# Kernel tuning notes

Measured on AMD Instinct MI355X. Metric: run time of the kernel, lower is better.

The kernel has to match this reference:

```python
import jax, jax.numpy as jnp
import numpy as np

NEG = -1e9
BN_EPS = 1e-3  # keras BatchNormalization default epsilon
LRELU = 0.2    # GAT leaky-relu slope


def _gat(Xt, bias_mat, Wg, a1, a2, bg):
    """Dense multi-head GAT (Velickovic TF impl).
    Xt: [B,N,F], bias_mat: [B,N,N] additive mask (0 / -1e9).
    Wg: [H,F,D], a1/a2/bg: [H,D]. Returns [B,N,H*D]."""
    feats = jnp.einsum('bnf,hfd->bhnd', Xt, Wg)          # [B,H,N,D]
    f1 = jnp.einsum('bhnd,hd->bhn', feats, a1)
    f2 = jnp.einsum('bhnd,hd->bhn', feats, a2)
    logits = f1[:, :, :, None] + f2[:, :, None, :]        # [B,H,N,N]
    logits = jax.nn.leaky_relu(logits, LRELU) + bias_mat[:, None]
    coefs = jax.nn.softmax(logits, axis=-1)
    vals = jnp.einsum('bhnm,bhmd->bhnd', coefs, feats) + bg[None, :, None, :]
    vals = jax.nn.elu(vals)
    B, H, N, D = vals.shape
    return jnp.transpose(vals, (0, 2, 1, 3)).reshape(B, N, H * D)


def setup_inputs() -> dict:
    key = jax.random.key(0)
    ks = jax.random.split(key, 16)
    B, T, N, F = 4, 12, 2048, 64
    H, D = 4, 16           # attn_heads, hid_units
    C = H * D              # out_channels = 64

    X = jax.random.normal(ks[0], (B, T, N, F), dtype=jnp.float32)
    # random sparse adjacency (~avg degree 16) + self loops -> additive mask
    adj = jax.random.uniform(ks[1], (B, N, N)) < (16.0 / N)
    adj = adj | jnp.eye(N, dtype=bool)[None]
    bias_mat = jnp.where(adj, 0.0, NEG).astype(jnp.float32)

    he = lambda k, s: jax.random.normal(k, s, dtype=jnp.float32) * np.sqrt(2.0 / s[-2] if len(s) > 1 else 2.0 / s[-1])
    return {
        'X': X, 'bias_mat': bias_mat,
        'W_z': he(ks[2], (F, C)), 'Z_bias': he(ks[3], (1, C)),
        'W_h': he(ks[4], (F, C)), 'H_bias': he(ks[5], (1, C)),
        'Wg_z': he(ks[6], (H, F, D)), 'a1_z': he(ks[7], (H, D)),
        'a2_z': he(ks[8], (H, D)), 'bg_z': jnp.zeros((H, D), jnp.float32),
        'Wg_h': he(ks[9], (H, F, D)), 'a1_h': he(ks[10], (H, D)),
        'a2_h': he(ks[11], (H, D)), 'bg_h': jnp.zeros((H, D), jnp.float32),
        'bn_gamma': jnp.ones((C,), jnp.float32), 'bn_beta': jnp.zeros((C,), jnp.float32),
        'bn_mean': jnp.zeros((C,), jnp.float32), 'bn_var': jnp.ones((C,), jnp.float32),
    }


def reference(X, bias_mat, W_z, Z_bias, W_h, H_bias,
              Wg_z, a1_z, a2_z, bg_z, Wg_h, a1_h, a2_h, bg_h,
              bn_gamma, bn_beta, bn_mean, bn_var):
    B, T, N, F = X.shape
    C = W_z.shape[1]
    H0 = jnp.zeros((B, N, C), dtype=jnp.float32)

    def step(Hc, Xt):
        Z = _gat(Xt, bias_mat, Wg_z, a1_z, a2_z, bg_z) + Xt @ W_z + Z_bias + Hc
        Z = jax.nn.sigmoid(Z)
        Tt = _gat(Xt, bias_mat, Wg_h, a1_h, a2_h, bg_h) + Hc + Xt @ W_h + H_bias
        Tt = jnp.tanh(Tt)
        Hn = Z * Hc + (1.0 - Z) * Tt
        return Hn, None

    Xs = jnp.transpose(X, (1, 0, 2, 3))  # [T,B,N,F]
    Hf, _ = jax.lax.scan(step, H0, Xs)
    # last_layer=True path: BatchNorm (inference, moving stats) on final H
    out = (Hf - bn_mean) * jax.lax.rsqrt(bn_var + BN_EPS) * bn_gamma + bn_beta
    return out
```

## Files before the change

### kernel.cpp

```cpp
#include <hip/hip_runtime.h>
#include <cstdint>
#include <cstddef>

#define NB 4
#define NT 12
#define NN 2048
#define NF 64
#define NH 4
#define ND 16
#define NC 64
#define MAXD 64
#define NR (NB * NT * NN)

typedef _Float16 f16x8 __attribute__((ext_vector_type(8)));
typedef _Float16 f16x2 __attribute__((ext_vector_type(2)));
typedef float f32x4 __attribute__((ext_vector_type(4)));

#define LR(v) ((v) >= 0.f ? (v) : 0.2f * (v))
#define RCPF(x) __builtin_amdgcn_rcpf(x)

#define MACLO(acc, w, d)                                                      \
  asm("v_fma_mix_f32 %0, %1, %2, %0 op_sel:[0,0,0] op_sel_hi:[0,1,0]"         \
      : "+v"(acc) : "v"(w), "v"(d))
#define MACHI(acc, w, d)                                                      \
  asm("v_fma_mix_f32 %0, %1, %2, %0 op_sel:[0,1,0] op_sel_hi:[0,1,0]"         \
      : "+v"(acc) : "v"(w), "v"(d))

__global__ __launch_bounds__(256) void build_adj_k(const float* __restrict__ bias,
                                                   int* __restrict__ adj,
                                                   int* __restrict__ deg) {
  int gtid = blockIdx.x * 256 + threadIdx.x;
  int wid = gtid >> 6;
  int lane = threadIdx.x & 63;
  if (wid >= NB * NN) return;
  const float* row = bias + (size_t)wid * NN;
  int* arow = adj + (size_t)wid * MAXD;
  int count = 0;
  for (int c0 = 0; c0 < NN; c0 += 64) {
    float v = __builtin_nontemporal_load(row + c0 + lane);
    bool e = (v > -1e8f);
    unsigned long long m = __ballot(e);
    int pre = __popcll(m & ((1ull << lane) - 1ull));
    if (e) {
      int pos = count + pre;
      if (pos < MAXD) arow[pos] = c0 + lane;
    }
    count += __popcll(m);
  }
  if (lane == 0) deg[wid] = count < MAXD ? count : MAXD;
}

__global__ __launch_bounds__(256) void prep_w_k(
    const float* __restrict__ Wgz, const float* __restrict__ Wgh,
    const float* __restrict__ Wz,  const float* __restrict__ Wh,
    const float* __restrict__ a1z, const float* __restrict__ a2z,
    const float* __restrict__ a1h, const float* __restrict__ a2h,
    const float* __restrict__ Zb,  const float* __restrict__ Hb,
    _Float16* __restrict__ W16, float* __restrict__ biasC) {
  int idx = blockIdx.x * 256 + threadIdx.x;
  if (idx < 272 * 64) {
    int c = idx >> 6, k = idx & 63;
    float w;
    if (c < 64)       w = Wgz[((c >> 4) << 10) + (k << 4) + (c & 15)];
    else if (c < 128) { int q = c - 64; w = Wgh[((q >> 4) << 10) + (k << 4) + (q & 15)]; }
    else if (c < 192) w = Wz[(k << 6) + (c - 128)];
    else if (c < 256) w = Wh[(k << 6) + (c - 192)];
    else {
      int j = c - 256, h = j & 3;
      const float* Wg = (j & 4) ? Wgh : Wgz;
      const float* av = (j & 8) ? ((j & 4) ? a2h : a2z) : ((j & 4) ? a1h : a1z);
      float s = 0.f;
#pragma unroll
      for (int d = 0; d < 16; d++)
        s = fmaf(Wg[(h << 10) + (k << 4) + d], av[(h << 4) + d], s);
      w = s;
    }
    W16[idx] = (_Float16)w;
  }
  if (blockIdx.x == 0 && threadIdx.x < 128)
    biasC[threadIdx.x] =
        (threadIdx.x < 64) ? Zb[threadIdx.x] : Hb[threadIdx.x - 64];
}

__global__ __launch_bounds__(256) void mfma_gemm_k(
    const float* __restrict__ X, const _Float16* __restrict__ W16,
    const float* __restrict__ biasC,
    uint32_t* __restrict__ gbufF, uint32_t* __restrict__ gbufS,
    float* __restrict__ fbuf) {
  __shared__ uint32_t tr[4][16 * 68];
  const int tid = threadIdx.x;
  const int wv = tid >> 6, lane = tid & 63;
  const int m = lane & 15, quad = lane >> 4;
  const unsigned rw = blockIdx.x * 64 + wv * 16;
  uint32_t* tw = tr[wv];

  const float* xr = X + (size_t)(rw + m) * 64;
  float4 x0 = *(const float4*)(xr + quad * 8);
  float4 x1 = *(const float4*)(xr + quad * 8 + 4);
  float4 x2 = *(const float4*)(xr + 32 + quad * 8);
  float4 x3 = *(const float4*)(xr + 32 + quad * 8 + 4);
  f16x8 A0 = {(_Float16)x0.x, (_Float16)x0.y, (_Float16)x0.z, (_Float16)x0.w,
              (_Float16)x1.x, (_Float16)x1.y, (_Float16)x1.z, (_Float16)x1.w};
  f16x8 A1 = {(_Float16)x2.x, (_Float16)x2.y, (_Float16)x2.z, (_Float16)x2.w,
              (_Float16)x3.x, (_Float16)x3.y, (_Float16)x3.z, (_Float16)x3.w};

  float bzc[4], bhc[4];
#pragma unroll
  for (int j = 0; j < 4; j++) {
    bzc[j] = biasC[j * 16 + m];
    bhc[j] = biasC[64 + j * 16 + m];
  }
  const int rsub = lane >> 4, chk = lane & 15;

  f32x4 zacc[4], zs[4];
#pragma unroll
  for (int ct = 0; ct < 17; ct++) {
    const _Float16* wp = W16 + (ct * 16 + m) * 64;
    f16x8 B0 = *(const f16x8*)(wp + quad * 8);
    f16x8 B1 = *(const f16x8*)(wp + 32 + quad * 8);
    f32x4 acc = {0.f, 0.f, 0.f, 0.f};
    acc = __builtin_amdgcn_mfma_f32_16x16x32_f16(A0, B0, acc, 0, 0, 0);
    acc = __builtin_amdgcn_mfma_f32_16x16x32_f16(A1, B1, acc, 0, 0, 0);
    if (ct < 4) {
      zacc[ct] = acc;
    } else if (ct < 8) {
      const int j = ct - 4;
#pragma unroll
      for (int r = 0; r < 4; r++) {
        f16x2 pv = {(_Float16)zacc[j][r], (_Float16)acc[r]};
        tw[(quad * 4 + r) * 68 + j * 16 + m] = __builtin_bit_cast(uint32_t, pv);
      }
      if (ct == 7) {
#pragma unroll
        for (int i = 0; i < 4; i++) {
          int row = i * 4 + rsub;
          uint4 v = *(const uint4*)&tw[row * 68 + chk * 4];
          *(uint4*)&gbufF[(size_t)(rw + row) * 64 + chk * 4] = v;
        }
      }
    } else if (ct < 12) {
#pragma unroll
      for (int r = 0; r < 4; r++) zs[ct - 8][r] = acc[r] + bzc[ct - 8];
    } else if (ct < 16) {
      const int j = ct - 12;
#pragma unroll
      for (int r = 0; r < 4; r++) {
        f16x2 pv = {(_Float16)zs[j][r], (_Float16)(acc[r] + bhc[j])};
        tw[(quad * 4 + r) * 68 + j * 16 + m] = __builtin_bit_cast(uint32_t, pv);
      }
      if (ct == 15) {
#pragma unroll
        for (int i = 0; i < 4; i++) {
          int row = i * 4 + rsub;
          uint4 v = *(const uint4*)&tw[row * 68 + chk * 4];
          *(uint4*)&gbufS[(size_t)(rw + row) * 64 + chk * 4] = v;
        }
      }
    } else {
      const unsigned rb = rw + quad * 4;
#pragma unroll
      for (int r = 0; r < 4; r++) fbuf[(size_t)(rb + r) * 16 + m] = acc[r];
    }
  }
}

__global__ __launch_bounds__(256) void attn_gru_k(
    const uint32_t* __restrict__ gbufF, const uint32_t* __restrict__ gbufS,
    const float* __restrict__ fbuf,
    const int* __restrict__ adj, const int* __restrict__ deg,
    const float* __restrict__ bgz, const float* __restrict__ bgh,
    const float* __restrict__ gam, const float* __restrict__ bet,
    const float* __restrict__ mu, const float* __restrict__ var,
    float* __restrict__ out) {
  __shared__ int adjL[4][MAXD];
  __shared__ float wexp[4][8][68];
  const int tid = threadIdx.x;
  const int lane = tid & 63;
  const int ws = tid >> 6;
  const int node = blockIdx.x * 4 + ws;
  const int b = node >> 11;
  const int nl = node & (NN - 1);
  const int dg = deg[node];
  adjL[ws][lane] = (lane < dg) ? adj[node * MAXD + lane] : 0;
  const int dgp = (dg + 3) & ~3;
  const int ch = lane, hh = lane >> 4;
  const int sr = lane & 7, ss = lane >> 3;

#pragma unroll
  for (int k = 0; k < 8; k++) wexp[ws][k][lane] = 0.f;

  const float bz = bgz[ch], bh = bgh[ch];
  const float bnm = mu[ch];
  const float bns = rsqrtf(var[ch] + 1e-3f);
  const float bng = gam[ch], bnb = bet[ch];

  float hc = 0.f;
#pragma unroll 1
  for (int t = 0; t < NT; t++) {
    const unsigned rb = (unsigned)(b * NT + t) * NN;
    const float* fb = fbuf + (size_t)rb * 16;
    const uint32_t* gF = gbufF + (size_t)rb * 64;
    const uint32_t* gS = gbufS + (size_t)rb * 64;

    {
      const float4* p = (const float4*)(fb + nl * 16);
      float4 f1z = p[0], f1h = p[1];
      if (lane < dg) {
        int mm = adjL[ws][lane];
        const float4* q = (const float4*)(fb + mm * 16);
        float4 f2z = q[2], f2h = q[3];
        wexp[ws][0][lane] = __expf(LR(f1z.x + f2z.x));
        wexp[ws][1][lane] = __expf(LR(f1z.y + f2z.y));
        wexp[ws][2][lane] = __expf(LR(f1z.z + f2z.z));
        wexp[ws][3][lane] = __expf(LR(f1z.w + f2z.w));
        wexp[ws][4][lane] = __expf(LR(f1h.x + f2h.x));
        wexp[ws][5][lane] = __expf(LR(f1h.y + f2h.y));
        wexp[ws][6][lane] = __expf(LR(f1h.z + f2h.z));
        wexp[ws][7][lane] = __expf(LR(f1h.w + f2h.w));
      }
    }

    float4 u0 = *(const float4*)&wexp[ws][sr][ss * 8];
    float4 u1 = *(const float4*)&wexp[ws][sr][ss * 8 + 4];
    float part = ((u0.x + u0.y) + (u0.z + u0.w)) +
                 ((u1.x + u1.y) + (u1.z + u1.w));
    part += __shfl_xor(part, 8);
    part += __shfl_xor(part, 16);
    part += __shfl_xor(part, 32);
    const float rsz = RCPF(__shfl(part, hh));
    const float rsh = RCPF(__shfl(part, 4 + hh));

    float az = 0.f, ah = 0.f;
    const float* wz = wexp[ws][hh];
    const float* wh = wexp[ws][4 + hh];
    for (int mi = 0; mi < dgp; mi += 4) {
      int4 ma = *(const int4*)&adjL[ws][mi];
      float4 wza = *(const float4*)&wz[mi];
      float4 wha = *(const float4*)&wh[mi];
      uint32_t d0 = gF[(ma.x << 6) + ch];
      uint32_t d1 = gF[(ma.y << 6) + ch];
      uint32_t d2 = gF[(ma.z << 6) + ch];
      uint32_t d3 = gF[(ma.w << 6) + ch];
      MACLO(az, wza.x, d0); MACHI(ah, wha.x, d0);
      MACLO(az, wza.y, d1); MACHI(ah, wha.y, d1);
      MACLO(az, wza.z, d2); MACHI(ah, wha.z, d2);
      MACLO(az, wza.w, d3); MACHI(ah, wha.w, d3);
    }
    az *= rsz;
    ah *= rsh;

    f16x2 sp = __builtin_bit_cast(f16x2, gS[(nl << 6) + ch]);
    float vz = az + bz; vz = vz > 0.f ? vz : __expf(vz) - 1.f;
    float vh = ah + bh; vh = vh > 0.f ? vh : __expf(vh) - 1.f;
    float zp = vz + (float)sp.x + hc;
    float tp = vh + (float)sp.y + hc;
    float zg = RCPF(1.f + __expf(-zp));
    float tg = 1.f - 2.f * RCPF(__expf(2.f * tp) + 1.f);
    hc = zg * hc + (1.f - zg) * tg;
  }

  out[(size_t)node * 64 + ch] = (hc - bnm) * bns * bng + bnb;
}

extern "C" void kernel_launch(void* const* d_in, const int* in_sizes, int n_in,
                              void* d_out, int out_size, void* d_ws, size_t ws_size,
                              hipStream_t stream) {
  (void)in_sizes; (void)n_in; (void)out_size; (void)ws_size;
  const float* X   = (const float*)d_in[0];
  const float* bm  = (const float*)d_in[1];
  const float* Wz  = (const float*)d_in[2];
  const float* Zb  = (const float*)d_in[3];
  const float* Wh  = (const float*)d_in[4];
  const float* Hb  = (const float*)d_in[5];
  const float* Wgz = (const float*)d_in[6];
  const float* a1z = (const float*)d_in[7];
  const float* a2z = (const float*)d_in[8];
  const float* bgz = (const float*)d_in[9];
  const float* Wgh = (const float*)d_in[10];
  const float* a1h = (const float*)d_in[11];
  const float* a2h = (const float*)d_in[12];
  const float* bgh = (const float*)d_in[13];
  const float* gam = (const float*)d_in[14];
  const float* bet = (const float*)d_in[15];
  const float* mu  = (const float*)d_in[16];
  const float* var = (const float*)d_in[17];
  float* out = (float*)d_out;

  char* p = (char*)d_ws;
  uint32_t* gbufF = (uint32_t*)p; p += (size_t)NR * 64 * sizeof(uint32_t);
  uint32_t* gbufS = (uint32_t*)p; p += (size_t)NR * 64 * sizeof(uint32_t);
  float*    fbuf  = (float*)p;    p += (size_t)NR * 16 * sizeof(float);
  int*      adj   = (int*)p;      p += (size_t)NB * NN * MAXD * sizeof(int);
  int*      deg   = (int*)p;      p += (size_t)NB * NN * sizeof(int);
  _Float16* W16   = (_Float16*)p; p += 272 * 64 * sizeof(_Float16);
  float*    biasC = (float*)p;    p += 128 * sizeof(float);

  prep_w_k<<<dim3(68), dim3(256), 0, stream>>>(
      Wgz, Wgh, Wz, Wh, a1z, a2z, a1h, a2h, Zb, Hb, W16, biasC);
  build_adj_k<<<dim3(NB * NN / 4), dim3(256), 0, stream>>>(bm, adj, deg);
  mfma_gemm_k<<<dim3(NR / 64), dim3(256), 0, stream>>>(
      X, W16, biasC, gbufF, gbufS, fbuf);
  attn_gru_k<<<dim3(NB * NN / 4), dim3(256), 0, stream>>>(
      gbufF, gbufS, fbuf, adj, deg, bgz, bgh, gam, bet, mu, var, out);
}
```

Baseline: 243.2 us.

## Prefetch next-step attention scalars, swizzle block order, unroll neighbor gather by 8

The attention-GRU kernel now loads the f1/f2 attention scalars for step t+1 while step t is being computed, so that global latency is hidden across timesteps. The skip-term load is issued early. The neighbor gather loop is unrolled to 8 neighbors per iteration to keep more loads in flight. Block IDs are also swizzled so adjacent blocks map to nodes spread across the graph, and the BatchNorm parameter loads move after the loop. The trade-off is higher register pressure and a remainder-handling path in the gather loop.

```diff
diff --git a/kernel.cpp b/kernel.cpp
--- a/kernel.cpp
+++ b/kernel.cpp
@@ -177,11 +177,14 @@
   const int tid = threadIdx.x;
   const int lane = tid & 63;
   const int ws = tid >> 6;
-  const int node = blockIdx.x * 4 + ws;
+  const int bid = blockIdx.x;
+  const int swz = (bid & 7) * (2048 / 8) + (bid >> 3);
+  const int node = swz * 4 + ws;
   const int b = node >> 11;
   const int nl = node & (NN - 1);
   const int dg = deg[node];
-  adjL[ws][lane] = (lane < dg) ? adj[node * MAXD + lane] : 0;
+  const int myadj = (lane < dg) ? adj[node * MAXD + lane] : 0;
+  adjL[ws][lane] = myadj;
   const int dgp = (dg + 3) & ~3;
   const int ch = lane, hh = lane >> 4;
   const int sr = lane & 7, ss = lane >> 3;
@@ -190,34 +193,46 @@
   for (int k = 0; k < 8; k++) wexp[ws][k][lane] = 0.f;
 
   const float bz = bgz[ch], bh = bgh[ch];
-  const float bnm = mu[ch];
-  const float bns = rsqrtf(var[ch] + 1e-3f);
-  const float bng = gam[ch], bnb = bet[ch];
+
+  float4 c1z, c1h, c2z, c2h;
+  {
+    const float* fb0 = fbuf + (size_t)(b * NT) * NN * 16;
+    const float4* p0 = (const float4*)(fb0 + nl * 16);
+    const float4* q0 = (const float4*)(fb0 + (size_t)myadj * 16);
+    c1z = p0[0]; c1h = p0[1]; c2z = q0[2]; c2h = q0[3];
+  }
 
   float hc = 0.f;
 #pragma unroll 1
   for (int t = 0; t < NT; t++) {
     const unsigned rb = (unsigned)(b * NT + t) * NN;
-    const float* fb = fbuf + (size_t)rb * 16;
     const uint32_t* gF = gbufF + (size_t)rb * 64;
-    const uint32_t* gS = gbufS + (size_t)rb * 64;
-
-    {
-      const float4* p = (const float4*)(fb + nl * 16);
-      float4 f1z = p[0], f1h = p[1];
-      if (lane < dg) {
-        int mm = adjL[ws][lane];
-        const float4* q = (const float4*)(fb + mm * 16);
-        float4 f2z = q[2], f2h = q[3];
-        wexp[ws][0][lane] = __expf(LR(f1z.x + f2z.x));
-        wexp[ws][1][lane] = __expf(LR(f1z.y + f2z.y));
-        wexp[ws][2][lane] = __expf(LR(f1z.z + f2z.z));
-        wexp[ws][3][lane] = __expf(LR(f1z.w + f2z.w));
-        wexp[ws][4][lane] = __expf(LR(f1h.x + f2h.x));
-        wexp[ws][5][lane] = __expf(LR(f1h.y + f2h.y));
-        wexp[ws][6][lane] = __expf(LR(f1h.z + f2h.z));
-        wexp[ws][7][lane] = __expf(LR(f1h.w + f2h.w));
-      }
+    const uint32_t spd = gbufS[((size_t)rb + nl) * 64 + ch];
+
+    float e0 = __expf(LR(c1z.x + c2z.x));
+    float e1 = __expf(LR(c1z.y + c2z.y));
+    float e2 = __expf(LR(c1z.z + c2z.z));
+    float e3 = __expf(LR(c1z.w + c2z.w));
+    float e4 = __expf(LR(c1h.x + c2h.x));
+    float e5 = __expf(LR(c1h.y + c2h.y));
+    float e6 = __expf(LR(c1h.z + c2h.z));
+    float e7 = __expf(LR(c1h.w + c2h.w));
+    if (lane < dg) {
+      wexp[ws][0][lane] = e0;
+      wexp[ws][1][lane] = e1;
+      wexp[ws][2][lane] = e2;
+      wexp[ws][3][lane] = e3;
+      wexp[ws][4][lane] = e4;
+      wexp[ws][5][lane] = e5;
+      wexp[ws][6][lane] = e6;
+      wexp[ws][7][lane] = e7;
+    }
+
+    if (t + 1 < NT) {
+      const float* fbn = fbuf + ((size_t)rb + NN) * 16;
+      const float4* pn = (const float4*)(fbn + nl * 16);
+      const float4* qn = (const float4*)(fbn + (size_t)myadj * 16);
+      c1z = pn[0]; c1h = pn[1]; c2z = qn[2]; c2h = qn[3];
     }
 
     float4 u0 = *(const float4*)&wexp[ws][sr][ss * 8];
@@ -233,23 +248,48 @@
     float az = 0.f, ah = 0.f;
     const float* wz = wexp[ws][hh];
     const float* wh = wexp[ws][4 + hh];
-    for (int mi = 0; mi < dgp; mi += 4) {
+    int mi = 0;
+    for (; mi + 8 <= dgp; mi += 8) {
       int4 ma = *(const int4*)&adjL[ws][mi];
-      float4 wza = *(const float4*)&wz[mi];
-      float4 wha = *(const float4*)&wh[mi];
+      int4 mb = *(const int4*)&adjL[ws][mi + 4];
       uint32_t d0 = gF[(ma.x << 6) + ch];
       uint32_t d1 = gF[(ma.y << 6) + ch];
       uint32_t d2 = gF[(ma.z << 6) + ch];
       uint32_t d3 = gF[(ma.w << 6) + ch];
+      uint32_t d4 = gF[(mb.x << 6) + ch];
+      uint32_t d5 = gF[(mb.y << 6) + ch];
+      uint32_t d6 = gF[(mb.z << 6) + ch];
+      uint32_t d7 = gF[(mb.w << 6) + ch];
+      float4 wza = *(const float4*)&wz[mi];
+      float4 wzb = *(const float4*)&wz[mi + 4];
+      float4 wha = *(const float4*)&wh[mi];
+      float4 whb = *(const float4*)&wh[mi + 4];
       MACLO(az, wza.x, d0); MACHI(ah, wha.x, d0);
       MACLO(az, wza.y, d1); MACHI(ah, wha.y, d1);
       MACLO(az, wza.z, d2); MACHI(ah, wha.z, d2);
       MACLO(az, wza.w, d3); MACHI(ah, wha.w, d3);
+      MACLO(az, wzb.x, d4); MACHI(ah, whb.x, d4);
+      MACLO(az, wzb.y, d5); MACHI(ah, whb.y, d5);
+      MACLO(az, wzb.z, d6); MACHI(ah, whb.z, d6);
+      MACLO(az, wzb.w, d7); MACHI(ah, whb.w, d7);
+    }
+    if (mi < dgp) {
+      int4 ma = *(const int4*)&adjL[ws][mi];
+      uint32_t d0 = gF[(ma.x << 6) + ch];
+      uint32_t d1 = gF[(ma.y << 6) + ch];
+      uint32_t d2 = gF[(ma.z << 6) + ch];
+      uint32_t d3 = gF[(ma.w << 6) + ch];
+      float4 wza = *(const float4*)&wz[mi];
+      float4 wha = *(const float4*)&wh[mi];
+      MACLO(az, wza.x, d0); MACHI(ah, wha.x, d0);
+      MACLO(az, wza.y, d1); MACHI(ah, wha.y, d1);
+      MACLO(az, wza.z, d2); MACHI(ah, wha.z, d2);
+      MACLO(az, wza.w, d3); MACHI(ah, wha.w, d3);
     }
     az *= rsz;
     ah *= rsh;
 
-    f16x2 sp = __builtin_bit_cast(f16x2, gS[(nl << 6) + ch]);
+    f16x2 sp = __builtin_bit_cast(f16x2, spd);
     float vz = az + bz; vz = vz > 0.f ? vz : __expf(vz) - 1.f;
     float vh = ah + bh; vh = vh > 0.f ? vh : __expf(vh) - 1.f;
     float zp = vz + (float)sp.x + hc;
@@ -259,7 +299,9 @@
     hc = zg * hc + (1.f - zg) * tg;
   }
 
-  out[(size_t)node * 64 + ch] = (hc - bnm) * bns * bng + bnb;
+  const float bnm = mu[ch];
+  const float bns = rsqrtf(var[ch] + 1e-3f);
+  out[(size_t)node * 64 + ch] = (hc - bnm) * bns * gam[ch] + bet[ch];
 }
 
 extern "C" void kernel_launch(void* const* d_in, const int* in_sizes, int n_in,
```

New measurement: 238.0 us. 2.2% less time.

## Split attention from GRU recurrence to parallelize attention across timesteps

Applied to the files above, without the earlier changes.

The fused attention+GRU kernel, which looped serially over 12 timesteps per node, is split in two. An attention kernel runs over a (nodes, T) grid and writes fp16 pre-activations to a new workspace buffer, and a light elementwise GRU kernel then runs the recurrence. This exposes 12x more parallel work for the gather-heavy attention stage. The cost is an extra global write and read of an fp16 intermediate plus one more launch. It also unrolls the neighbor gather loop by 8, pre-shifts adjacency indices, and uses fmaxf for leaky relu.

```diff
diff --git a/kernel.cpp b/kernel.cpp
--- a/kernel.cpp
+++ b/kernel.cpp
@@ -16,7 +16,7 @@
 typedef _Float16 f16x2 __attribute__((ext_vector_type(2)));
 typedef float f32x4 __attribute__((ext_vector_type(4)));
 
-#define LR(v) ((v) >= 0.f ? (v) : 0.2f * (v))
+#define LR(v) fmaxf((v), 0.2f * (v))
 #define RCPF(x) __builtin_amdgcn_rcpf(x)
 
 #define MACLO(acc, w, d)                                                      \
@@ -164,102 +164,133 @@
   }
 }
 
-__global__ __launch_bounds__(256) void attn_gru_k(
+__global__ __launch_bounds__(256) void attn_k(
     const uint32_t* __restrict__ gbufF, const uint32_t* __restrict__ gbufS,
     const float* __restrict__ fbuf,
     const int* __restrict__ adj, const int* __restrict__ deg,
     const float* __restrict__ bgz, const float* __restrict__ bgh,
-    const float* __restrict__ gam, const float* __restrict__ bet,
-    const float* __restrict__ mu, const float* __restrict__ var,
-    float* __restrict__ out) {
-  __shared__ int adjL[4][MAXD];
+    uint32_t* __restrict__ abuf) {
+  __shared__ int adjS[4][MAXD];
   __shared__ float wexp[4][8][68];
   const int tid = threadIdx.x;
   const int lane = tid & 63;
   const int ws = tid >> 6;
   const int node = blockIdx.x * 4 + ws;
+  const int t = blockIdx.y;
   const int b = node >> 11;
   const int nl = node & (NN - 1);
   const int dg = deg[node];
-  adjL[ws][lane] = (lane < dg) ? adj[node * MAXD + lane] : 0;
+  adjS[ws][lane] = (lane < dg) ? (adj[node * MAXD + lane] << 6) : 0;
   const int dgp = (dg + 3) & ~3;
   const int ch = lane, hh = lane >> 4;
   const int sr = lane & 7, ss = lane >> 3;
 
-#pragma unroll
-  for (int k = 0; k < 8; k++) wexp[ws][k][lane] = 0.f;
-
-  const float bz = bgz[ch], bh = bgh[ch];
-  const float bnm = mu[ch];
-  const float bns = rsqrtf(var[ch] + 1e-3f);
-  const float bng = gam[ch], bnb = bet[ch];
-
+  const unsigned rb = (unsigned)(b * NT + t) * NN;
+  const float* fb = fbuf + (size_t)rb * 16;
+  const uint32_t* gF = gbufF + (size_t)rb * 64;
+  const uint32_t spd = gbufS[((size_t)rb + nl) * 64 + ch];
+
+  {
+    const float4* p = (const float4*)(fb + nl * 16);
+    float4 f1z = p[0], f1h = p[1];
+    if (lane < dg) {
+      const float4* q =
+          (const float4*)((const char*)fb + (size_t)(unsigned)adjS[ws][lane]);
+      float4 f2z = q[2], f2h = q[3];
+      wexp[ws][0][lane] = __expf(LR(f1z.x + f2z.x));
+      wexp[ws][1][lane] = __expf(LR(f1z.y + f2z.y));
+      wexp[ws][2][lane] = __expf(LR(f1z.z + f2z.z));
+      wexp[ws][3][lane] = __expf(LR(f1z.w + f2z.w));
+      wexp[ws][4][lane] = __expf(LR(f1h.x + f2h.x));
+      wexp[ws][5][lane] = __expf(LR(f1h.y + f2h.y));
+      wexp[ws][6][lane] = __expf(LR(f1h.z + f2h.z));
+      wexp[ws][7][lane] = __expf(LR(f1h.w + f2h.w));
+    } else {
+#pragma unroll
+      for (int k = 0; k < 8; k++) wexp[ws][k][lane] = 0.f;
+    }
+  }
+
+  float4 u0 = *(const float4*)&wexp[ws][sr][ss * 8];
+  float4 u1 = *(const float4*)&wexp[ws][sr][ss * 8 + 4];
+  float part = ((u0.x + u0.y) + (u0.z + u0.w)) +
+               ((u1.x + u1.y) + (u1.z + u1.w));
+  part += __shfl_xor(part, 8);
+  part += __shfl_xor(part, 16);
+  part += __shfl_xor(part, 32);
+  const float rsz = RCPF(__shfl(part, hh));
+  const float rsh = RCPF(__shfl(part, 4 + hh));
+
+  float az = 0.f, ah = 0.f;
+  const float* wz = wexp[ws][hh];
+  const float* wh = wexp[ws][4 + hh];
+  int mi = 0;
+  for (; mi + 8 <= dgp; mi += 8) {
+    int4 ma = *(const int4*)&adjS[ws][mi];
+    int4 mb = *(const int4*)&adjS[ws][mi + 4];
+    uint32_t d0 = gF[ma.x + ch];
+    uint32_t d1 = gF[ma.y + ch];
+    uint32_t d2 = gF[ma.z + ch];
+    uint32_t d3 = gF[ma.w + ch];
+    uint32_t d4 = gF[mb.x + ch];
+    uint32_t d5 = gF[mb.y + ch];
+    uint32_t d6 = gF[mb.z + ch];
+    uint32_t d7 = gF[mb.w + ch];
+    float4 wza = *(const float4*)&wz[mi];
+    float4 wzb = *(const float4*)&wz[mi + 4];
+    float4 wha = *(const float4*)&wh[mi];
+    float4 whb = *(const float4*)&wh[mi + 4];
+    MACLO(az, wza.x, d0); MACHI(ah, wha.x, d0);
+    MACLO(az, wza.y, d1); MACHI(ah, wha.y, d1);
+    MACLO(az, wza.z, d2); MACHI(ah, wha.z, d2);
+    MACLO(az, wza.w, d3); MACHI(ah, wha.w, d3);
+    MACLO(az, wzb.x, d4); MACHI(ah, whb.x, d4);
+    MACLO(az, wzb.y, d5); MACHI(ah, whb.y, d5);
+    MACLO(az, wzb.z, d6); MACHI(ah, whb.z, d6);
+    MACLO(az, wzb.w, d7); MACHI(ah, whb.w, d7);
+  }
+  if (mi < dgp) {
+    int4 ma = *(const int4*)&adjS[ws][mi];
+    uint32_t d0 = gF[ma.x + ch];
+    uint32_t d1 = gF[ma.y + ch];
+    uint32_t d2 = gF[ma.z + ch];
+    uint32_t d3 = gF[ma.w + ch];
+    float4 wza = *(const float4*)&wz[mi];
+    float4 wha = *(const float4*)&wh[mi];
+    MACLO(az, wza.x, d0); MACHI(ah, wha.x, d0);
+    MACLO(az, wza.y, d1); MACHI(ah, wha.y, d1);
+    MACLO(az, wza.z, d2); MACHI(ah, wha.z, d2);
+    MACLO(az, wza.w, d3); MACHI(ah, wha.w, d3);
+  }
+  az *= rsz;
+  ah *= rsh;
+
+  f16x2 sp = __builtin_bit_cast(f16x2, spd);
+  float vz = az + bgz[ch]; vz = vz > 0.f ? vz : __expf(vz) - 1.f;
+  float vh = ah + bgh[ch]; vh = vh > 0.f ? vh : __expf(vh) - 1.f;
+  f16x2 pre = {(_Float16)(vz + (float)sp.x), (_Float16)(vh + (float)sp.y)};
+  abuf[(size_t)(rb + nl) * 64 + ch] = __builtin_bit_cast(uint32_t, pre);
+}
+
+__global__ __launch_bounds__(256) void gru_k(
+    const uint32_t* __restrict__ abuf,
+    const float* __restrict__ gam, const float* __restrict__ bet,
+    const float* __restrict__ mu, const float* __restrict__ var,
+    float* __restrict__ out) {
+  const int gtid = blockIdx.x * 256 + threadIdx.x;
+  const int node = gtid >> 6, ch = gtid & 63;
+  const int b = node >> 11, nl = node & (NN - 1);
   float hc = 0.f;
-#pragma unroll 1
+#pragma unroll
   for (int t = 0; t < NT; t++) {
-    const unsigned rb = (unsigned)(b * NT + t) * NN;
-    const float* fb = fbuf + (size_t)rb * 16;
-    const uint32_t* gF = gbufF + (size_t)rb * 64;
-    const uint32_t* gS = gbufS + (size_t)rb * 64;
-
-    {
-      const float4* p = (const float4*)(fb + nl * 16);
-      float4 f1z = p[0], f1h = p[1];
-      if (lane < dg) {
-        int mm = adjL[ws][lane];
-        const float4* q = (const float4*)(fb + mm * 16);
-        float4 f2z = q[2], f2h = q[3];
-        wexp[ws][0][lane] = __expf(LR(f1z.x + f2z.x));
-        wexp[ws][1][lane] = __expf(LR(f1z.y + f2z.y));
-        wexp[ws][2][lane] = __expf(LR(f1z.z + f2z.z));
-        wexp[ws][3][lane] = __expf(LR(f1z.w + f2z.w));
-        wexp[ws][4][lane] = __expf(LR(f1h.x + f2h.x));
-        wexp[ws][5][lane] = __expf(LR(f1h.y + f2h.y));
-        wexp[ws][6][lane] = __expf(LR(f1h.z + f2h.z));
-        wexp[ws][7][lane] = __expf(LR(f1h.w + f2h.w));
-      }
-    }
-
-    float4 u0 = *(const float4*)&wexp[ws][sr][ss * 8];
-    float4 u1 = *(const float4*)&wexp[ws][sr][ss * 8 + 4];
-    float part = ((u0.x + u0.y) + (u0.z + u0.w)) +
-                 ((u1.x + u1.y) + (u1.z + u1.w));
-    part += __shfl_xor(part, 8);
-    part += __shfl_xor(part, 16);
-    part += __shfl_xor(part, 32);
-    const float rsz = RCPF(__shfl(part, hh));
-    const float rsh = RCPF(__shfl(part, 4 + hh));
-
-    float az = 0.f, ah = 0.f;
-    const float* wz = wexp[ws][hh];
-    const float* wh = wexp[ws][4 + hh];
-    for (int mi = 0; mi < dgp; mi += 4) {
-      int4 ma = *(const int4*)&adjL[ws][mi];
-      float4 wza = *(const float4*)&wz[mi];
-      float4 wha = *(const float4*)&wh[mi];
-      uint32_t d0 = gF[(ma.x << 6) + ch];
-      uint32_t d1 = gF[(ma.y << 6) + ch];
-      uint32_t d2 = gF[(ma.z << 6) + ch];
-      uint32_t d3 = gF[(ma.w << 6) + ch];
-      MACLO(az, wza.x, d0); MACHI(ah, wha.x, d0);
-      MACLO(az, wza.y, d1); MACHI(ah, wha.y, d1);
-      MACLO(az, wza.z, d2); MACHI(ah, wha.z, d2);
-      MACLO(az, wza.w, d3); MACHI(ah, wha.w, d3);
-    }
-    az *= rsz;
-    ah *= rsh;
-
-    f16x2 sp = __builtin_bit_cast(f16x2, gS[(nl << 6) + ch]);
-    float vz = az + bz; vz = vz > 0.f ? vz : __expf(vz) - 1.f;
-    float vh = ah + bh; vh = vh > 0.f ? vh : __expf(vh) - 1.f;
-    float zp = vz + (float)sp.x + hc;
-    float tp = vh + (float)sp.y + hc;
-    float zg = RCPF(1.f + __expf(-zp));
-    float tg = 1.f - 2.f * RCPF(__expf(2.f * tp) + 1.f);
+    f16x2 pre = __builtin_bit_cast(
+        f16x2, abuf[(size_t)((b * NT + t) * NN + nl) * 64 + ch]);
+    float zg = RCPF(1.f + __expf(-((float)pre.x + hc)));
+    float ta = (float)pre.y + hc;
+    float tg = 1.f - 2.f * RCPF(__expf(2.f * ta) + 1.f);
     hc = zg * hc + (1.f - zg) * tg;
   }
-
-  out[(size_t)node * 64 + ch] = (hc - bnm) * bns * bng + bnb;
+  out[gtid] = (hc - mu[ch]) * rsqrtf(var[ch] + 1e-3f) * gam[ch] + bet[ch];
 }
 
 extern "C" void kernel_launch(void* const* d_in, const int* in_sizes, int n_in,
@@ -290,6 +321,7 @@
   uint32_t* gbufF = (uint32_t*)p; p += (size_t)NR * 64 * sizeof(uint32_t);
   uint32_t* gbufS = (uint32_t*)p; p += (size_t)NR * 64 * sizeof(uint32_t);
   float*    fbuf  = (float*)p;    p += (size_t)NR * 16 * sizeof(float);
+  uint32_t* abuf  = (uint32_t*)p; p += (size_t)NR * 64 * sizeof(uint32_t);
   int*      adj   = (int*)p;      p += (size_t)NB * NN * MAXD * sizeof(int);
   int*      deg   = (int*)p;      p += (size_t)NB * NN * sizeof(int);
   _Float16* W16   = (_Float16*)p; p += 272 * 64 * sizeof(_Float16);
@@ -300,6 +332,8 @@
   build_adj_k<<<dim3(NB * NN / 4), dim3(256), 0, stream>>>(bm, adj, deg);
   mfma_gemm_k<<<dim3(NR / 64), dim3(256), 0, stream>>>(
       X, W16, biasC, gbufF, gbufS, fbuf);
-  attn_gru_k<<<dim3(NB * NN / 4), dim3(256), 0, stream>>>(
-      gbufF, gbufS, fbuf, adj, deg, bgz, bgh, gam, bet, mu, var, out);
-}
+  attn_k<<<dim3(NB * NN / 4, NT), dim3(256), 0, stream>>>(
+      gbufF, gbufS, fbuf, adj, deg, bgz, bgh, abuf);
+  gru_k<<<dim3(NB * NN * 64 / 256), dim3(256), 0, stream>>>(
+      abuf, gam, bet, mu, var, out);
+}
```

New measurement: 240.8 us. Within noise of the previous version (-1.0%).
